# Performance work log

Hardware: AMD Instinct MI355X
Metric: run time of the kernel (lower is better)

The kernel has to match this reference:

```python
import jax, jax.numpy as jnp
import numpy as np

THRESHOLD = 0.15  # init kwarg


def setup_inputs() -> dict:
    key = jax.random.key(0)
    B, T, N = 64, 1024, 512
    inputs = jax.random.normal(key, (B, T, N), dtype=jnp.float32)
    return {"inputs": inputs}


def reference(inputs) -> jnp.ndarray:
    # inputs: [B, T, N]; Pearson correlation across the sample (time) axis.
    B, T, N = inputs.shape
    xc = inputs - jnp.mean(inputs, axis=1, keepdims=True)        # [B,T,N]
    cov = jnp.einsum('bti,btj->bij', xc, xc)                     # [B,N,N] (unnormalized; norm cancels)
    d = jnp.sqrt(jnp.diagonal(cov, axis1=1, axis2=2))            # [B,N]
    corr = cov / (d[:, :, None] * d[:, None, :])                 # [B,N,N]

    # Original loop: for i<j, if |corr[:,i,j]|>thr: mask = mask * one_hot(i).
    # Equivalent closed form: let fired[b,i] = any_{j>i} |corr[b,i,j]|>thr.
    #   0 fired rows -> all-ones mask
    #   1 fired row  -> one_hot of that i (repeated onehot(i) multiplies are idempotent)
    #   >=2 distinct fired rows -> onehot(i1)*onehot(i2)=0 -> all-zeros mask
    upper = jnp.triu(jnp.ones((N, N), dtype=bool), k=1)
    cond = (jnp.abs(corr) > THRESHOLD) & upper                   # [B,N,N]
    fired = jnp.any(cond, axis=2)                                # [B,N]
    num_fired = jnp.sum(fired, axis=1)                           # [B]

    ones = jnp.ones((B, N), dtype=jnp.float32)
    mask = jnp.where((num_fired == 0)[:, None], ones,
                     jnp.where((num_fired == 1)[:, None],
                               fired.astype(jnp.float32),
                               jnp.zeros_like(ones)))
    return mask
```

## Files before the change

### kernel.cpp

```cpp
#include <hip/hip_runtime.h>
#include <hip/hip_bf16.h>

#define BB 64
#define TT 1024
#define NN 512
#define LISTCAP (1u << 18)

static constexpr float THR = 0.15f;
static constexpr float SQ    = 6.0f / 127.0f;
static constexpr float INVSQ = 127.0f / 6.0f;

typedef __attribute__((ext_vector_type(4))) int i32x4;

__device__ __forceinline__ void gload16(const void* g, void* lds_dst) {
    __builtin_amdgcn_global_load_lds(
        (const __attribute__((address_space(1))) unsigned int*)g,
        (__attribute__((address_space(3))) unsigned int*)lds_dst, 16, 0, 0);
}

__global__ __launch_bounds__(512) void transpose_colsum(
    const float* __restrict__ x, char* __restrict__ xq,
    float* __restrict__ s1, float* __restrict__ dv,
    float* __restrict__ nv, float* __restrict__ nl,
    unsigned* __restrict__ fired, unsigned* __restrict__ cnt) {
    __shared__ uint4 tile[2048];
    __shared__ float red[3][8][64];
    int b = blockIdx.x, ng = blockIdx.y;
    int n0 = ng * 64;
    int tid = threadIdx.x, w = tid >> 6, l = tid & 63;
    const float* xb = x + (size_t)b * TT * NN + n0 + l;
    float a1 = 0.f, a2 = 0.f, al = 0.f;
    if (b == 0 && ng == 0 && tid == 64) *cnt = 0;

    unsigned sw4 = ((((unsigned)w >> 1) ^ (((unsigned)l >> 1) & 3u)) & 3u);
    unsigned wroff = (unsigned)l * 64u + (sw4 << 4) + ((unsigned)(w & 1)) * 8u;

    for (int tc = 0; tc < 2; ++tc) {
        #pragma unroll
        for (int i = 0; i < 8; ++i) {
            int t0 = tc * 512 + i * 64 + w * 8;
            unsigned lo = 0, hi = 0;
            #pragma unroll
            for (int j = 0; j < 8; ++j) {
                float v = xb[(size_t)(t0 + j) * NN];
                a1 += v;
                a2 = fmaf(v, v, a2);
                int q = __float2int_rn(v * INVSQ);
                q = q > 127 ? 127 : (q < -127 ? -127 : q);
                float lr = fmaf((float)q, -SQ, v);
                al = fmaf(lr, lr, al);
                unsigned byte = (unsigned)(q & 255);
                if (j < 4) lo |= byte << (8 * j);
                else       hi |= byte << (8 * (j - 4));
            }
            *(uint2*)((char*)tile + i * 4096 + wroff) = make_uint2(lo, hi);
        }
        __syncthreads();
        {
            const char* src = (const char*)tile + w * 4096 + l * 16;
            char* dst = xq + ((size_t)((b * 8 + ng) * 16) + tc * 8 + w) * 4096 + l * 16;
            #pragma unroll
            for (int it = 0; it < 4; ++it)
                *(uint4*)(dst + (size_t)it * 1024) =
                    *(const uint4*)(src + (size_t)it * 1024);
        }
        __syncthreads();
    }
    red[0][w][l] = a1; red[1][w][l] = a2; red[2][w][l] = al;
    __syncthreads();
    if (tid < 64) {
        float r1 = 0.f, r2 = 0.f, rl = 0.f;
        #pragma unroll
        for (int k = 0; k < 8; ++k) {
            r1 += red[0][k][tid]; r2 += red[1][k][tid]; rl += red[2][k][tid];
        }
        size_t o = (size_t)b * NN + n0 + tid;
        s1[o] = r1;
        dv[o] = r2 - r1 * r1 * (1.0f / TT);
        nv[o] = sqrtf(r2);
        nl[o] = sqrtf(rl);
        fired[o] = 0u;
    }
}

__global__ __launch_bounds__(256, 8) void corr_mfma(
    const char* __restrict__ xq, const float* __restrict__ s1,
    const float* __restrict__ dv, const float* __restrict__ nv,
    const float* __restrict__ nl, unsigned* __restrict__ fired,
    unsigned* __restrict__ cnt, unsigned* __restrict__ list) {
    __shared__ uint4 ldsbuf[1024];
    char* base = (char*)ldsbuf;

    int id = blockIdx.x;
    int swz = ((id & 7) * 288) + (id >> 3);
    int b = swz / 36;
    int u = swz % 36;
    int ti = 0, rem = u;
    while (rem >= (8 - ti)) { rem -= (8 - ti); ++ti; }
    int tj = ti + rem;
    int i0 = ti * 64, j0 = tj * 64;
    bool diag = (ti == tj);

    int tid = threadIdx.x;
    int wave = tid >> 6, lane = tid & 63;
    int rl = lane & 15, kg = lane >> 4;

    const char* srcA = xq + ((size_t)(b * 8 + ti) * 16) * 4096 + tid * 16;
    const char* srcB = xq + ((size_t)(b * 8 + tj) * 16) * 4096 + tid * 16;

    auto STAGE = [&](int s, int buf) {
        char* d = base + (buf << 13) + wave * 1024;
        gload16(srcA + (size_t)s * 4096, d);
        if (!diag) gload16(srcB + (size_t)s * 4096, d + 4096);
    };

    int wr = wave >> 1, wc = wave & 1;
    bool skip_mm = diag && (wr == 1) && (wc == 0);

    unsigned aoff[2], boff[2];
    #pragma unroll
    for (int f = 0; f < 2; ++f) {
        unsigned ca = (unsigned)(32 * wr + 16 * f + rl);
        aoff[f] = ca * 64u + ((((unsigned)kg ^ ((ca >> 1) & 3u)) & 3u) << 4);
        unsigned cb2 = (unsigned)(32 * wc + 16 * f + rl);
        boff[f] = cb2 * 64u + ((((unsigned)kg ^ ((cb2 >> 1) & 3u)) & 3u) << 4);
    }
    unsigned bbase = diag ? 0u : 4096u;

    i32x4 acc[2][2];
    #pragma unroll
    for (int i = 0; i < 2; ++i)
        #pragma unroll
        for (int j = 0; j < 2; ++j)
            acc[i][j] = (i32x4)0;

    STAGE(0, 0);
    __syncthreads();

    for (int it = 0; it < 16; ++it) {
        if (it + 1 < 16) STAGE(it + 1, (it + 1) & 1);
        const char* cb = base + ((it & 1) << 13);
        if (!skip_mm) {
            i32x4 A[2], Bv[2];
            #pragma unroll
            for (int f = 0; f < 2; ++f) A[f] = *(const i32x4*)(cb + aoff[f]);
            #pragma unroll
            for (int f = 0; f < 2; ++f) Bv[f] = *(const i32x4*)(cb + bbase + boff[f]);
            #pragma unroll
            for (int fj = 0; fj < 2; ++fj)
                #pragma unroll
                for (int fi = 0; fi < 2; ++fi)
                    acc[fi][fj] = __builtin_amdgcn_mfma_i32_16x16x64_i8(
                        A[fi], Bv[fj], acc[fi][fj], 0, 0, 0);
        }
        __syncthreads();
    }

    const float thr2 = THR * THR;
    const float invT = 1.0f / TT;
    const float s2 = SQ * SQ;
    const float* s1b = s1 + (size_t)b * NN;
    const float* dvb = dv + (size_t)b * NN;
    const float* nvb = nv + (size_t)b * NN;
    const float* nlb = nl + (size_t)b * NN;
    unsigned* fb = fired + (size_t)b * NN;
    int rowb = i0 + 32 * wr + kg * 4;
    int colb = j0 + 32 * wc + rl;
    #pragma unroll
    for (int fj = 0; fj < 2; ++fj) {
        int gj = colb + 16 * fj;
        float sj = s1b[gj], djv = dvb[gj];
        float nvj = nvb[gj], nlj = nlb[gj];
        #pragma unroll
        for (int fi = 0; fi < 2; ++fi) {
            int gi0 = rowb + 16 * fi;
            #pragma unroll
            for (int r = 0; r < 4; ++r) {
                int gi = gi0 + r;
                if (gj > gi) {
                    float cc = s2 * (float)acc[fi][fj][r] - s1b[gi] * sj * invT;
                    float lim = thr2 * dvb[gi] * djv;
                    float nvi = nvb[gi], nli = nlb[gi];
                    float B = nli * nvj + nlj * nvi + 3.0f * nli * nlj
                              + 1e-3f * nvi * nvj;
                    float a = fabsf(cc);
                    float lo = a - B;
                    if (lo > 0.0f && lo * lo > lim) {
                        atomicOr(&fb[gi], 1u);
                    } else if ((a + B) * (a + B) > lim) {
                        unsigned idx = atomicAdd(cnt, 1u);
                        if (idx < LISTCAP)
                            list[idx] = ((unsigned)b << 18) | ((unsigned)gi << 9)
                                        | (unsigned)gj;
                    }
                }
            }
        }
    }
}

__global__ __launch_bounds__(256) void cleanup_pairs(
    const float* __restrict__ x, const float* __restrict__ s1,
    const float* __restrict__ dv, const unsigned* __restrict__ cnt,
    const unsigned* __restrict__ list, unsigned* __restrict__ fired) {
    unsigned n = *cnt;
    if (n > LISTCAP) n = LISTCAP;
    int lane = threadIdx.x & 63;
    int gw = (blockIdx.x * 256 + threadIdx.x) >> 6;
    int nw = (gridDim.x * 256) >> 6;
    for (unsigned p = gw; p < n; p += nw) {
        unsigned e = list[p];
        int b = e >> 18, i = (e >> 9) & 511, j = e & 511;
        const float* xb = x + (size_t)b * TT * NN;
        double s = 0.0;
        for (int t = lane; t < TT; t += 64)
            s += (double)xb[(size_t)t * NN + i] * (double)xb[(size_t)t * NN + j];
        #pragma unroll
        for (int o = 32; o > 0; o >>= 1)
            s += __shfl_xor(s, o, 64);
        if (lane == 0) {
            double cov = s - (double)s1[(size_t)b * NN + i]
                             * (double)s1[(size_t)b * NN + j] / (double)TT;
            double lim = (double)THR * (double)THR
                         * (double)dv[(size_t)b * NN + i]
                         * (double)dv[(size_t)b * NN + j];
            if (cov * cov > lim) atomicOr(&fired[(size_t)b * NN + i], 1u);
        }
    }
}

__global__ __launch_bounds__(512) void finalize_mask(
    const unsigned* __restrict__ fired, float* __restrict__ out) {
    int b = blockIdx.x;
    int n = threadIdx.x;
    unsigned f = fired[(size_t)b * NN + n];
    __shared__ int wsum[8];
    unsigned long long m = __ballot(f != 0u);
    int lane = n & 63;
    int w = n >> 6;
    if (lane == 0) wsum[w] = __popcll(m);
    __syncthreads();
    int cnt = 0;
    #pragma unroll
    for (int i = 0; i < 8; ++i) cnt += wsum[i];
    float val = (cnt == 0) ? 1.0f : ((cnt == 1) ? (f ? 1.0f : 0.0f) : 0.0f);
    out[(size_t)b * NN + n] = val;
}

extern "C" void kernel_launch(void* const* d_in, const int* in_sizes, int n_in,
                              void* d_out, int out_size, void* d_ws, size_t ws_size,
                              hipStream_t stream) {
    const float* x = (const float*)d_in[0];
    float* out = (float*)d_out;

    char* xq = (char*)d_ws;
    float* s1 = (float*)(xq + (size_t)BB * NN * TT);
    float* dv = s1 + (size_t)BB * NN;
    float* nv = dv + (size_t)BB * NN;
    float* nl = nv + (size_t)BB * NN;
    unsigned* fired = (unsigned*)(nl + (size_t)BB * NN);
    unsigned* cnt   = fired + (size_t)BB * NN;
    unsigned* list  = cnt + 16;

    transpose_colsum<<<dim3(BB, 8), 512, 0, stream>>>(x, xq, s1, dv, nv, nl,
                                                      fired, cnt);
    corr_mfma<<<dim3(2304), 256, 0, stream>>>(xq, s1, dv, nv, nl, fired, cnt, list);
    cleanup_pairs<<<128, 256, 0, stream>>>(x, s1, dv, cnt, list, fired);
    finalize_mask<<<BB, 512, 0, stream>>>(fired, out);
}
```

Before: 92.15 us.

## Split preprocessing into bf16 transpose pass plus separate int8 quantization kernel

```diff
diff --git a/kernel.cpp b/kernel.cpp
--- a/kernel.cpp
+++ b/kernel.cpp
@@ -19,50 +19,51 @@
 }
 
 __global__ __launch_bounds__(512) void transpose_colsum(
-    const float* __restrict__ x, char* __restrict__ xq,
+    const float* __restrict__ x, ushort* __restrict__ xbf,
     float* __restrict__ s1, float* __restrict__ dv,
     float* __restrict__ nv, float* __restrict__ nl,
     unsigned* __restrict__ fired, unsigned* __restrict__ cnt) {
-    __shared__ uint4 tile[2048];
+    __shared__ ushort tile[64 * 512];
     __shared__ float red[3][8][64];
     int b = blockIdx.x, ng = blockIdx.y;
     int n0 = ng * 64;
     int tid = threadIdx.x, w = tid >> 6, l = tid & 63;
-    const float* xb = x + (size_t)b * TT * NN + n0 + l;
+    const float* xb = x + (size_t)b * TT * NN;
     float a1 = 0.f, a2 = 0.f, al = 0.f;
+    unsigned swz = ((unsigned)l & 7u) << 4;
+
     if (b == 0 && ng == 0 && tid == 64) *cnt = 0;
 
-    unsigned sw4 = ((((unsigned)w >> 1) ^ (((unsigned)l >> 1) & 3u)) & 3u);
-    unsigned wroff = (unsigned)l * 64u + (sw4 << 4) + ((unsigned)(w & 1)) * 8u;
-
     for (int tc = 0; tc < 2; ++tc) {
-        #pragma unroll
         for (int i = 0; i < 8; ++i) {
-            int t0 = tc * 512 + i * 64 + w * 8;
-            unsigned lo = 0, hi = 0;
-            #pragma unroll
-            for (int j = 0; j < 8; ++j) {
-                float v = xb[(size_t)(t0 + j) * NN];
-                a1 += v;
-                a2 = fmaf(v, v, a2);
-                int q = __float2int_rn(v * INVSQ);
-                q = q > 127 ? 127 : (q < -127 ? -127 : q);
-                float lr = fmaf((float)q, -SQ, v);
-                al = fmaf(lr, lr, al);
-                unsigned byte = (unsigned)(q & 255);
-                if (j < 4) lo |= byte << (8 * j);
-                else       hi |= byte << (8 * (j - 4));
+            int tl0 = i * 64 + w * 8;
+            int t0 = tc * 512 + tl0;
+            unsigned hp[4];
+            #pragma unroll
+            for (int q = 0; q < 4; ++q) {
+                float v0 = xb[(size_t)(t0 + 2 * q) * NN + n0 + l];
+                float v1 = xb[(size_t)(t0 + 2 * q + 1) * NN + n0 + l];
+                a1 += v0 + v1;
+                a2 += v0 * v0 + v1 * v1;
+                unsigned u0 = __float_as_uint(v0), u1 = __float_as_uint(v1);
+                float h0 = __uint_as_float(u0 & 0xFFFF0000u);
+                float h1 = __uint_as_float(u1 & 0xFFFF0000u);
+                float l0 = v0 - h0, l1 = v1 - h1;
+                al += l0 * l0 + l1 * l1;
+                hp[q] = (u0 >> 16) | (u1 & 0xFFFF0000u);
             }
-            *(uint2*)((char*)tile + i * 4096 + wroff) = make_uint2(lo, hi);
+            unsigned off = (unsigned)l * 1024u + (((unsigned)tl0 * 2u) ^ swz);
+            *(uint4*)((char*)tile + off) = make_uint4(hp[0], hp[1], hp[2], hp[3]);
         }
         __syncthreads();
-        {
-            const char* src = (const char*)tile + w * 4096 + l * 16;
-            char* dst = xq + ((size_t)((b * 8 + ng) * 16) + tc * 8 + w) * 4096 + l * 16;
-            #pragma unroll
-            for (int it = 0; it < 4; ++it)
-                *(uint4*)(dst + (size_t)it * 1024) =
-                    *(const uint4*)(src + (size_t)it * 1024);
+        #pragma unroll
+        for (int cc = 0; cc < 8; ++cc) {
+            int cl = w * 8 + cc;
+            unsigned src = (unsigned)cl * 1024u
+                           + (((unsigned)l * 16u) ^ (((unsigned)cl & 7u) << 4));
+            uint4 val = *(const uint4*)((char*)tile + src);
+            ushort* dst = xbf + ((size_t)(b * NN + n0 + cl) * TT + tc * 512 + l * 8);
+            *(uint4*)dst = val;
         }
         __syncthreads();
     }
@@ -80,6 +81,75 @@
         nv[o] = sqrtf(r2);
         nl[o] = sqrtf(rl);
         fired[o] = 0u;
+    }
+}
+
+__global__ __launch_bounds__(512) void quant8(
+    const ushort* __restrict__ xbf, char* __restrict__ xq, float* __restrict__ nl) {
+    __shared__ float red[8][64];
+    int id = blockIdx.x;
+    int b = id >> 3, g = id & 7;
+    int tid = threadIdx.x, w = tid >> 6, l = tid & 63;
+    int c0 = l >> 2, sl = l & 3;
+    int kk = sl ^ ((c0 >> 1) & 3);
+
+    float rq2[4] = {0.f, 0.f, 0.f, 0.f};
+
+    #pragma unroll
+    for (int si = 0; si < 2; ++si) {
+        int s = w + 8 * si;
+        char* pbase = xq + ((size_t)((b * 8 + g) * 16) + s) * 4096;
+        #pragma unroll
+        for (int i2 = 0; i2 < 4; ++i2) {
+            int cp = c0 + 16 * i2;
+            const ushort* src = xbf + ((size_t)(b * NN + g * 64 + cp) * TT
+                                       + s * 64 + kk * 16);
+            ushort4 h0 = *(const ushort4*)(src);
+            ushort4 h1 = *(const ushort4*)(src + 4);
+            ushort4 h2 = *(const ushort4*)(src + 8);
+            ushort4 h3 = *(const ushort4*)(src + 12);
+            unsigned pw[4];
+            float racc = 0.f;
+            #pragma unroll
+            for (int qd = 0; qd < 4; ++qd) {
+                ushort4 hv = (qd == 0) ? h0 : (qd == 1) ? h1 : (qd == 2) ? h2 : h3;
+                unsigned pb = 0;
+                #pragma unroll
+                for (int j = 0; j < 4; ++j) {
+                    unsigned us = (j == 0) ? hv.x : (j == 1) ? hv.y
+                                  : (j == 2) ? hv.z : hv.w;
+                    float v = __uint_as_float(us << 16);
+                    int q = __float2int_rn(v * INVSQ);
+                    q = q > 127 ? 127 : (q < -127 ? -127 : q);
+                    float r = fmaf((float)q, -SQ, v);
+                    racc = fmaf(r, r, racc);
+                    pb |= ((unsigned)(q & 255)) << (8 * j);
+                }
+                pw[qd] = pb;
+            }
+            rq2[i2] += racc;
+            *(uint4*)(pbase + i2 * 1024 + l * 16) =
+                make_uint4(pw[0], pw[1], pw[2], pw[3]);
+        }
+    }
+
+    #pragma unroll
+    for (int i2 = 0; i2 < 4; ++i2) {
+        rq2[i2] += __shfl_xor(rq2[i2], 1, 64);
+        rq2[i2] += __shfl_xor(rq2[i2], 2, 64);
+    }
+    if (sl == 0) {
+        #pragma unroll
+        for (int i2 = 0; i2 < 4; ++i2)
+            red[w][16 * i2 + c0] = rq2[i2];
+    }
+    __syncthreads();
+    if (tid < 64) {
+        float t = 0.f;
+        #pragma unroll
+        for (int k = 0; k < 8; ++k) t += red[k][tid];
+        size_t o = (size_t)b * NN + g * 64 + tid;
+        nl[o] = nl[o] + sqrtf(t);
     }
 }
 
@@ -253,7 +323,8 @@
     const float* x = (const float*)d_in[0];
     float* out = (float*)d_out;
 
-    char* xq = (char*)d_ws;
+    ushort* xbf = (ushort*)d_ws;
+    char* xq = (char*)(xbf + (size_t)BB * NN * TT);
     float* s1 = (float*)(xq + (size_t)BB * NN * TT);
     float* dv = s1 + (size_t)BB * NN;
     float* nv = dv + (size_t)BB * NN;
@@ -262,8 +333,9 @@
     unsigned* cnt   = fired + (size_t)BB * NN;
     unsigned* list  = cnt + 16;
 
-    transpose_colsum<<<dim3(BB, 8), 512, 0, stream>>>(x, xq, s1, dv, nv, nl,
+    transpose_colsum<<<dim3(BB, 8), 512, 0, stream>>>(x, xbf, s1, dv, nv, nl,
                                                       fired, cnt);
+    quant8<<<dim3(512), 512, 0, stream>>>(xbf, xq, nl);
     corr_mfma<<<dim3(2304), 256, 0, stream>>>(xq, s1, dv, nv, nl, fired, cnt, list);
     cleanup_pairs<<<128, 256, 0, stream>>>(x, s1, dv, cnt, list, fired);
     finalize_mask<<<BB, 512, 0, stream>>>(fired, out);
```

New measurement: 154.2 us. 67.3% more time.
